# Kernel tuning notes

Hardware: AMD Instinct MI355X
Metric: run time of the kernel (lower is better)

## Reference

```python
import jax, jax.numpy as jnp
import numpy as np

N = 4194304  # number of 3D points (surfels)
H, W = 1024, 1280


def setup_inputs() -> dict:
    key = jax.random.key(0)
    k1, k2, k3 = jax.random.split(key, 3)
    # camera-frame points: x,y in [-0.5, 0.5], z (depth) in [0.5, 2.5]
    xy = jax.random.uniform(k1, (N, 2), dtype=jnp.float32, minval=-0.5, maxval=0.5)
    z = jax.random.uniform(k2, (N, 1), dtype=jnp.float32, minval=0.5, maxval=2.5)
    points = jnp.concatenate([xy, z], axis=-1)
    colors = jax.random.uniform(k3, (N, 3), dtype=jnp.float32)
    fx = fy = 1000.0
    K = jnp.array([[fx, 0.0, W / 2.0], [0.0, fy, H / 2.0], [0.0, 0.0, 1.0]],
                  dtype=jnp.float32)
    return {"points": points, "colors": colors, "K": K, "height": H, "width": W}


def reference(points, colors, K, height, width):
    # pcd2depth: pinhole projection with rounding
    fx, fy, cx, cy = K[0, 0], K[1, 1], K[0, 2], K[1, 2]
    z = points[:, 2]
    u = jnp.round(fx * points[:, 0] / z + cx).astype(jnp.int32)
    v = jnp.round(fy * points[:, 1] / z + cy).astype(jnp.int32)
    valid = (z > 0) & (u >= 0) & (u < width) & (v >= 0) & (v < height)
    n = points.shape[0]
    npix = height * width
    # sentinel pixel npix for invalid points
    flat = jnp.where(valid, v * width + u, npix)
    # far-to-near overwrite after depth_sort=True)
    order = jnp.argsort(jnp.where(valid, z, jnp.inf))  # ascending depth
    flat_sorted = flat[order]
    ranks = jnp.arange(n, dtype=jnp.int32)
    # per-pixel min rank (rank = position in depth-ascending order)
    win = jnp.full(npix + 1, n, dtype=jnp.int32).at[flat_sorted].min(ranks)
    win = win[:npix]
    has_point = win < n
    winner = order[jnp.minimum(win, n - 1)]  # point index per pixel
    img = jnp.where(has_point[:, None], colors[winner].astype(jnp.float32), 0.0)
    return img.reshape(height, width, 3)
```

## Files before the change

kernel.cpp:

```cpp
#include <hip/hip_runtime.h>
#include <stdint.h>

#define NPTS    4194304
#define IMG_H   1024
#define IMG_W   1280
#define NPIX    (IMG_H * IMG_W)

#define TW      160
#define TH      32
#define TILES_X (IMG_W / TW)
#define TILES_Y (IMG_H / TH)
#define NBINS   (TILES_X * TILES_Y)
#define TPIX    (TW * TH)

#define NBLK    768
#define TPB     256

#define CHUNK_Q ((NPTS / 4 + NBLK - 1) / NBLK)
#define CHUNK_P (CHUNK_Q * 4)
#define SSTRIDE CHUNK_P

static const unsigned long long KEY_SENTINEL = ~0ULL;


__device__ __forceinline__ bool project(float x, float y, float z,
                                        float fx, float fy, float cx, float cy,
                                        int& u, int& v) {
    float uf = rintf(fx * x / z + cx);
    float vf = rintf(fy * y / z + cy);
    bool valid = (z > 0.0f) &&
                 (uf >= 0.0f) && (uf < (float)IMG_W) &&
                 (vf >= 0.0f) && (vf < (float)IMG_H);
    u = (int)uf;
    v = (int)vf;
    return valid;
}

__device__ __forceinline__ unsigned int zc_of(float z) {
    unsigned int zb = __float_as_uint(z);
    unsigned int zc = zb - 0x3F000000u;
    if ((int)zc < 0) zc = 0;
    if (zc > 0x1FFFFFFu) zc = 0x1FFFFFFu;
    return zc;
}

__global__ __launch_bounds__(TPB) void pass_bin(
        const float4* __restrict__ pts4, const float* __restrict__ Kmat,
        unsigned int* __restrict__ cnt_off ,
        unsigned long long* __restrict__ grec ,
        int n_quads, int qchunk) {
    __shared__ unsigned long long srec[CHUNK_P];
    __shared__ unsigned int hist[NBINS];
    __shared__ unsigned int cur[NBINS];
    __shared__ unsigned int tsum[64];

    int t   = threadIdx.x;
    int blk = blockIdx.x;
    if (t < NBINS) hist[t] = 0;
    __syncthreads();

    float fx = Kmat[0], cx = Kmat[2];
    float fy = Kmat[4], cy = Kmat[5];

    int q0 = blk * qchunk;
    int q1 = min(n_quads, q0 + qchunk);

    for (int q = q0 + t; q < q1; q += TPB) {
        float4 a = pts4[3 * q + 0];
        float4 b = pts4[3 * q + 1];
        float4 c = pts4[3 * q + 2];
        float px[4] = {a.x, a.w, b.z, c.y};
        float py[4] = {a.y, b.x, b.w, c.z};
        float pz[4] = {a.z, b.y, c.x, c.w};
#pragma unroll
        for (int k = 0; k < 4; ++k) {
            int u, v;
            if (project(px[k], py[k], pz[k], fx, fy, cx, cy, u, v)) {
                int bin = (v >> 5) * TILES_X + (u / TW);
                atomicAdd(&hist[bin], 1u);
            }
        }
    }
    __syncthreads();

    unsigned int hv[4];
    if (t < 64) {
#pragma unroll
        for (int j = 0; j < 4; ++j) hv[j] = hist[4 * t + j];
        tsum[t] = hv[0] + hv[1] + hv[2] + hv[3];
    }
    __syncthreads();
    for (int off = 1; off < 64; off <<= 1) {
        unsigned int x = 0;
        if (t < 64 && t >= off) x = tsum[t - off];
        __syncthreads();
        if (t < 64) tsum[t] += x;
        __syncthreads();
    }
    if (t < 64) {
        unsigned int run = (t > 0) ? tsum[t - 1] : 0u;
#pragma unroll
        for (int j = 0; j < 4; ++j) {
            cur[4 * t + j] = run;
            run += hv[j];
        }
    }
    __syncthreads();

    if (t < NBINS)
        cnt_off[(size_t)t * NBLK + blk] = (hist[t] << 16) | cur[t];
    __syncthreads();

    for (int q = q0 + t; q < q1; q += TPB) {
        float4 a = pts4[3 * q + 0];
        float4 b = pts4[3 * q + 1];
        float4 c = pts4[3 * q + 2];
        float px[4] = {a.x, a.w, b.z, c.y};
        float py[4] = {a.y, b.x, b.w, c.z};
        float pz[4] = {a.z, b.y, c.x, c.w};
        unsigned int i0 = 4u * (unsigned int)q;
#pragma unroll
        for (int k = 0; k < 4; ++k) {
            int u, v;
            if (project(px[k], py[k], pz[k], fx, fy, cx, cy, u, v)) {
                int tx  = u / TW;
                int bin = (v >> 5) * TILES_X + tx;
                unsigned int pos = (unsigned int)((v & 31) * TW + (u - tx * TW));
                unsigned int slot = atomicAdd(&cur[bin], 1u);
                srec[slot] = ((unsigned long long)pos << 47) |
                             ((unsigned long long)zc_of(pz[k]) << 22) |
                             (i0 + (unsigned int)k);
            }
        }
    }
    __syncthreads();

    unsigned int nrec = cur[NBINS - 1];
    unsigned long long* my = grec + (size_t)blk * SSTRIDE;
    for (unsigned int i = t; i < nrec; i += TPB) my[i] = srec[i];
}

__global__ __launch_bounds__(NBLK) void pass_render(
        const unsigned long long* __restrict__ grec,
        const unsigned int* __restrict__ cnt_off,
        const float* __restrict__ colors,
        float* __restrict__ out) {
    __shared__ unsigned long long key[TPIX];

    int t = threadIdx.x;
    int b = blockIdx.x;

    for (int i = t; i < TPIX; i += NBLK) key[i] = KEY_SENTINEL;

    unsigned int w   = cnt_off[(size_t)b * NBLK + t];
    unsigned int cnt = w >> 16;
    unsigned int off = w & 0xFFFFu;
    const unsigned long long* seg = grec + (size_t)t * SSTRIDE + off;
    __syncthreads();

    for (unsigned int r = 0; r < cnt; ++r) {
        unsigned long long rec = seg[r];
        unsigned int pos = (unsigned int)(rec >> 47);
        atomicMin(&key[pos], rec & ((1ULL << 47) - 1));
    }
    __syncthreads();

    int tx = b % TILES_X, ty = b / TILES_X;
    for (int i = t; i < TPIX; i += NBLK) {
        int row = i / TW, col = i - row * TW;
        unsigned long long kk = key[i];
        float r = 0.0f, g = 0.0f, bl = 0.0f;
        if (kk != KEY_SENTINEL) {
            unsigned int idx = (unsigned int)(kk & 0x3FFFFFu);
            r  = colors[3 * idx + 0];
            g  = colors[3 * idx + 1];
            bl = colors[3 * idx + 2];
        }
        size_t gp = (size_t)(ty * TH + row) * IMG_W + (size_t)(tx * TW + col);
        out[3 * gp + 0] = r;
        out[3 * gp + 1] = g;
        out[3 * gp + 2] = bl;
    }
}

__global__ void init_keys_vec(ulonglong2* __restrict__ keys, int n_vec2) {
    int i = blockIdx.x * blockDim.x + threadIdx.x;
    if (i < n_vec2) keys[i] = ulonglong2{~0ULL, ~0ULL};
}

__global__ void scatter_points_pretest(const float4* __restrict__ pts4,
                                       const float* __restrict__ Kmat,
                                       unsigned long long* __restrict__ keys,
                                       int n_quads) {
    int t = blockIdx.x * blockDim.x + threadIdx.x;
    if (t >= n_quads) return;
    float fx = Kmat[0], cx = Kmat[2];
    float fy = Kmat[4], cy = Kmat[5];
    float4 a = pts4[3 * t + 0];
    float4 b = pts4[3 * t + 1];
    float4 c = pts4[3 * t + 2];
    float px[4] = {a.x, a.w, b.z, c.y};
    float py[4] = {a.y, b.x, b.w, c.z};
    float pz[4] = {a.z, b.y, c.x, c.w};
    unsigned int i0 = 4u * (unsigned int)t;
#pragma unroll
    for (int k = 0; k < 4; ++k) {
        int u, v;
        if (!project(px[k], py[k], pz[k], fx, fy, cx, cy, u, v)) continue;
        int pix = v * IMG_W + u;
        unsigned long long key =
            ((unsigned long long)__float_as_uint(pz[k]) << 32) | (i0 + k);
        if (key < keys[pix]) atomicMin(&keys[pix], key);
    }
}

__global__ void resolve_pixels4(const unsigned long long* __restrict__ keys,
                                const float* __restrict__ colors,
                                float* __restrict__ out, int n_quads) {
    int t = blockIdx.x * blockDim.x + threadIdx.x;
    if (t >= n_quads) return;
    int base = 4 * t;
    ulonglong2 k01 = *(const ulonglong2*)(keys + base);
    ulonglong2 k23 = *(const ulonglong2*)(keys + base + 2);
    unsigned long long kk[4] = {k01.x, k01.y, k23.x, k23.y};
    float c[12];
#pragma unroll
    for (int j = 0; j < 4; ++j) {
        float r = 0.0f, g = 0.0f, b = 0.0f;
        if (kk[j] != KEY_SENTINEL) {
            unsigned int idx = (unsigned int)(kk[j] & 0xFFFFFFFFu);
            r = colors[3 * idx + 0];
            g = colors[3 * idx + 1];
            b = colors[3 * idx + 2];
        }
        c[3 * j + 0] = r; c[3 * j + 1] = g; c[3 * j + 2] = b;
    }
    float4* o = (float4*)(out + 3 * (size_t)base);
    o[0] = float4{c[0], c[1], c[2],  c[3]};
    o[1] = float4{c[4], c[5], c[6],  c[7]};
    o[2] = float4{c[8], c[9], c[10], c[11]};
}

extern "C" void kernel_launch(void* const* d_in, const int* in_sizes, int n_in,
                              void* d_out, int out_size, void* d_ws, size_t ws_size,
                              hipStream_t stream) {
    const float4* pts4  = (const float4*)d_in[0];
    const float* colors = (const float*)d_in[1];
    const float* Kmat   = (const float*)d_in[2];
    float* out = (float*)d_out;

    int n       = in_sizes[0] / 3;
    int n_quads = n / 4;
    int qchunk  = (n_quads + NBLK - 1) / NBLK;

    char* ws = (char*)d_ws;
    unsigned int*       cnt_off = (unsigned int*)ws;
    size_t tbl_bytes = (size_t)NBINS * NBLK * sizeof(unsigned int);
    unsigned long long* grec =
        (unsigned long long*)(ws + ((tbl_bytes + 63) & ~(size_t)63));
    size_t need = ((tbl_bytes + 63) & ~(size_t)63) +
                  (size_t)NBLK * SSTRIDE * sizeof(unsigned long long);

    if (qchunk <= CHUNK_Q && ws_size >= need) {
        pass_bin<<<NBLK, TPB, 0, stream>>>(pts4, Kmat, cnt_off, grec,
                                           n_quads, qchunk);
        pass_render<<<NBINS, NBLK, 0, stream>>>(grec, cnt_off, colors, out);
    } else {
        unsigned long long* keys = (unsigned long long*)d_ws;
        const int B = 256;
        int n_vec2 = NPIX / 2;
        init_keys_vec<<<(n_vec2 + B - 1) / B, B, 0, stream>>>(
            (ulonglong2*)keys, n_vec2);
        scatter_points_pretest<<<(n_quads + B - 1) / B, B, 0, stream>>>(
            pts4, Kmat, keys, n_quads);
        int npix_quads = NPIX / 4;
        resolve_pixels4<<<(npix_quads + B - 1) / B, B, 0, stream>>>(
            keys, colors, out, npix_quads);
    }
}
```

Before: 174.0 us.

## Shrink render tiles to 40x32 and use 256-thread render blocks

Render tiles narrow from 160 to 40 pixels wide, so there are 1024 bins instead of 256 and four times as many render blocks, each with a smaller shared key array. Each render block now has 256 threads, and each thread walks three bin-pass segments. The prefix scan in the bin pass now spans all 256 threads, and the count/offset table is stored block-major. The goal is more render parallelism and occupancy, at the cost of a larger offset table and more per-segment loop overhead.

```diff
diff --git a/kernel.cpp b/kernel.cpp
--- a/kernel.cpp
+++ b/kernel.cpp
@@ -6,7 +6,7 @@
 #define IMG_W   1280
 #define NPIX    (IMG_H * IMG_W)
 
-#define TW      160
+#define TW      40
 #define TH      32
 #define TILES_X (IMG_W / TW)
 #define TILES_Y (IMG_H / TH)
@@ -15,6 +15,7 @@
 
 #define NBLK    768
 #define TPB     256
+#define SEGS_PER_THREAD (NBLK / TPB)
 
 #define CHUNK_Q ((NPTS / 4 + NBLK - 1) / NBLK)
 #define CHUNK_P (CHUNK_Q * 4)
@@ -52,11 +53,12 @@
     __shared__ unsigned long long srec[CHUNK_P];
     __shared__ unsigned int hist[NBINS];
     __shared__ unsigned int cur[NBINS];
-    __shared__ unsigned int tsum[64];
+    __shared__ unsigned int tsum[TPB];
 
     int t   = threadIdx.x;
     int blk = blockIdx.x;
-    if (t < NBINS) hist[t] = 0;
+#pragma unroll
+    for (int i = t; i < NBINS; i += TPB) hist[i] = 0;
     __syncthreads();
 
     float fx = Kmat[0], cx = Kmat[2];
@@ -84,20 +86,19 @@
     __syncthreads();
 
     unsigned int hv[4];
-    if (t < 64) {
+    {
 #pragma unroll
         for (int j = 0; j < 4; ++j) hv[j] = hist[4 * t + j];
         tsum[t] = hv[0] + hv[1] + hv[2] + hv[3];
     }
     __syncthreads();
-    for (int off = 1; off < 64; off <<= 1) {
-        unsigned int x = 0;
-        if (t < 64 && t >= off) x = tsum[t - off];
+    for (int off = 1; off < TPB; off <<= 1) {
+        unsigned int x = (t >= off) ? tsum[t - off] : 0u;
         __syncthreads();
-        if (t < 64) tsum[t] += x;
+        tsum[t] += x;
         __syncthreads();
     }
-    if (t < 64) {
+    {
         unsigned int run = (t > 0) ? tsum[t - 1] : 0u;
 #pragma unroll
         for (int j = 0; j < 4; ++j) {
@@ -107,8 +108,9 @@
     }
     __syncthreads();
 
-    if (t < NBINS)
-        cnt_off[(size_t)t * NBLK + blk] = (hist[t] << 16) | cur[t];
+#pragma unroll
+    for (int i = t; i < NBINS; i += TPB)
+        cnt_off[(size_t)blk * NBINS + i] = (hist[i] << 16) | cur[i];
     __syncthreads();
 
     for (int q = q0 + t; q < q1; q += TPB) {
@@ -140,7 +142,7 @@
     for (unsigned int i = t; i < nrec; i += TPB) my[i] = srec[i];
 }
 
-__global__ __launch_bounds__(NBLK) void pass_render(
+__global__ __launch_bounds__(TPB) void pass_render(
         const unsigned long long* __restrict__ grec,
         const unsigned int* __restrict__ cnt_off,
         const float* __restrict__ colors,
@@ -150,23 +152,28 @@
     int t = threadIdx.x;
     int b = blockIdx.x;
 
-    for (int i = t; i < TPIX; i += NBLK) key[i] = KEY_SENTINEL;
-
-    unsigned int w   = cnt_off[(size_t)b * NBLK + t];
-    unsigned int cnt = w >> 16;
-    unsigned int off = w & 0xFFFFu;
-    const unsigned long long* seg = grec + (size_t)t * SSTRIDE + off;
-    __syncthreads();
-
-    for (unsigned int r = 0; r < cnt; ++r) {
-        unsigned long long rec = seg[r];
-        unsigned int pos = (unsigned int)(rec >> 47);
-        atomicMin(&key[pos], rec & ((1ULL << 47) - 1));
+#pragma unroll
+    for (int i = t; i < TPIX; i += TPB) key[i] = KEY_SENTINEL;
+    __syncthreads();
+
+#pragma unroll
+    for (int s = 0; s < SEGS_PER_THREAD; ++s) {
+        int blk = t + s * TPB;
+        unsigned int w   = cnt_off[(size_t)blk * NBINS + b];
+        unsigned int cnt = w >> 16;
+        unsigned int off = w & 0xFFFFu;
+        const unsigned long long* seg = grec + (size_t)blk * SSTRIDE + off;
+        for (unsigned int r = 0; r < cnt; ++r) {
+            unsigned long long rec = seg[r];
+            unsigned int pos = (unsigned int)(rec >> 47);
+            atomicMin(&key[pos], rec & ((1ULL << 47) - 1));
+        }
     }
     __syncthreads();
 
     int tx = b % TILES_X, ty = b / TILES_X;
-    for (int i = t; i < TPIX; i += NBLK) {
+#pragma unroll
+    for (int i = t; i < TPIX; i += TPB) {
         int row = i / TW, col = i - row * TW;
         unsigned long long kk = key[i];
         float r = 0.0f, g = 0.0f, bl = 0.0f;
@@ -255,7 +262,7 @@
 
     char* ws = (char*)d_ws;
     unsigned int*       cnt_off = (unsigned int*)ws;
-    size_t tbl_bytes = (size_t)NBINS * NBLK * sizeof(unsigned int);
+    size_t tbl_bytes = (size_t)NBLK * NBINS * sizeof(unsigned int);
     unsigned long long* grec =
         (unsigned long long*)(ws + ((tbl_bytes + 63) & ~(size_t)63));
     size_t need = ((tbl_bytes + 63) & ~(size_t)63) +
@@ -264,7 +271,7 @@
     if (qchunk <= CHUNK_Q && ws_size >= need) {
         pass_bin<<<NBLK, TPB, 0, stream>>>(pts4, Kmat, cnt_off, grec,
                                            n_quads, qchunk);
-        pass_render<<<NBINS, NBLK, 0, stream>>>(grec, cnt_off, colors, out);
+        pass_render<<<NBINS, TPB, 0, stream>>>(grec, cnt_off, colors, out);
     } else {
         unsigned long long* keys = (unsigned long long*)d_ws;
         const int B = 256;
```

Result: slower. 180.8 us (+3.9%).
